# Kernel optimization log

Measured on AMD Instinct MI355X. Metric: run time of the kernel, lower is better.

## Reference

```python
import jax, jax.numpy as jnp
import numpy as np

EPS = 1e-5
STRIDE = 4
NSAMPLE = 8


def _fps(p, m):
    # furthest point sampling on one cloud p:[n,3] -> int32 indices [m]
    d0 = jnp.sum((p - p[0]) ** 2, axis=-1)
    def step(dist, _):
        nxt = jnp.argmax(dist).astype(jnp.int32)
        d = jnp.sum((p - p[nxt]) ** 2, axis=-1)
        return jnp.minimum(dist, d), nxt
    _, idxs = jax.lax.scan(step, d0, None, length=m - 1)
    return jnp.concatenate([jnp.zeros((1,), jnp.int32), idxs])


def _bn(x, gamma, beta):
    # inference-mode BatchNorm1d with running_mean=0, running_var=1
    return gamma * x / jnp.sqrt(1.0 + EPS) + beta


def _transition_down(p, x, W, gamma, beta):
    # p:[B,n,3], x:[B,n,C]  (stride>1 path of TransitionDown)
    B, n, _ = p.shape
    m = n // STRIDE
    pc = jax.lax.stop_gradient(p)
    idx = jax.vmap(_fps, in_axes=(0, None))(pc, m)              # [B,m]
    n_p = jnp.take_along_axis(p, idx[:, :, None], axis=1)       # [B,m,3]
    npc = jax.lax.stop_gradient(n_p)
    # squared distances sampled->all points, [B,m,n] (no [B,m,n,3] temp)
    d2 = (jnp.sum(npc ** 2, -1)[:, :, None]
          + jnp.sum(pc ** 2, -1)[:, None, :]
          - 2.0 * jnp.einsum('bmd,bnd->bmn', npc, pc))
    _, knn = jax.lax.top_k(-d2, NSAMPLE)                        # [B,m,k]
    gp = jax.vmap(lambda pb, kb: pb[kb])(p, knn)                # [B,m,k,3]
    gx = jax.vmap(lambda xb, kb: xb[kb])(x, knn)                # [B,m,k,C]
    rel = gp - n_p[:, :, None, :]                               # use_xyz=True
    feat = jnp.concatenate([rel, gx], axis=-1)                  # [B,m,k,3+C]
    y = jax.nn.relu(_bn(feat @ W, gamma, beta))
    return n_p, jnp.max(y, axis=2)                              # MaxPool1d(k)


def setup_inputs():
    key = jax.random.key(0)
    ks = jax.random.split(key, 16)
    B, n = 8, 8192
    N = B * n
    inp = {
        'p0': jax.random.normal(ks[0], (N, 3), jnp.float32),
        'x0': jax.random.normal(ks[1], (N, 3), jnp.float32),
        'o0': (jnp.arange(1, B + 1) * n).astype(jnp.int32),
    }
    dims_in = [6, 3 + 32, 3 + 64, 3 + 128, 3 + 256]
    dims_out = [32, 64, 128, 256, 512]
    for i in range(5):
        s = 1.0 / np.sqrt(dims_in[i])
        inp[f'W{i+1}'] = jax.random.uniform(ks[2 + i], (dims_in[i], dims_out[i]), jnp.float32, -s, s)
        inp[f'g{i+1}'] = jnp.ones((dims_out[i],), jnp.float32)
        inp[f'b{i+1}'] = jnp.zeros((dims_out[i],), jnp.float32)
    s1 = 1.0 / np.sqrt(512.0)
    inp['Wc1'] = jax.random.uniform(ks[8], (512, 256), jnp.float32, -s1, s1)
    inp['bc1'] = jax.random.uniform(ks[9], (256,), jnp.float32, -s1, s1)
    inp['gcls'] = jnp.ones((256,), jnp.float32)
    inp['bcls'] = jnp.zeros((256,), jnp.float32)
    s2 = 1.0 / np.sqrt(256.0)
    inp['Wc2'] = jax.random.uniform(ks[10], (256, 40), jnp.float32, -s2, s2)
    inp['bc2'] = jax.random.uniform(ks[11], (40,), jnp.float32, -s2, s2)
    return inp


def reference(p0, x0, o0, W1, g1, b1, W2, g2, b2, W3, g3, b3, W4, g4, b4,
              W5, g5, b5, Wc1, bc1, gcls, bcls, Wc2, bc2):
    B = o0.shape[0]
    n = p0.shape[0] // B  # equal-size segments
    p = p0.reshape(B, n, 3)
    x = jnp.concatenate([p0, x0], axis=1).reshape(B, n, 6)  # c=6: cat(xyz, feat)
    # enc1: stride 1 -> relu(bn(linear(x)))
    x = jax.nn.relu(_bn(x @ W1, g1, b1))
    # enc2..enc5: FPS + KNN group + linear/bn/relu + maxpool over neighbors
    p, x = _transition_down(p, x, W2, g2, b2)
    p, x = _transition_down(p, x, W3, g3, b3)
    p, x = _transition_down(p, x, W4, g4, b4)
    p, x = _transition_down(p, x, W5, g5, b5)
    # offset-based segment mean pooling (equal segments -> mean over axis 1)
    pooled = jnp.mean(x, axis=1)                               # [B,512]
    h = jax.nn.relu(_bn(pooled @ Wc1 + bc1, gcls, bcls))       # dropout eval=id
    return h @ Wc2 + bc2                                       # [B,40]
```

## Files before the change

kernel.cpp:

```cpp
#include <hip/hip_runtime.h>
#include <float.h>

#define BNI 0.9999950000374997f

typedef unsigned int v2u __attribute__((ext_vector_type(2)));

__device__ __forceinline__ float sq3(float x, float y, float z) {
  return __fadd_rn(__fadd_rn(__fmul_rn(x, x), __fmul_rn(y, y)), __fmul_rn(z, z));
}

__device__ __forceinline__ int key_idx(double k) { return ~__double2loint(k); }

template <int CTRL>
__device__ __forceinline__ double dpp_max(double k) {
  union { double d; int i[2]; } u, r;
  u.d = k;
  r.i[0] = __builtin_amdgcn_mov_dpp(u.i[0], CTRL, 0xF, 0xF, true);
  r.i[1] = __builtin_amdgcn_mov_dpp(u.i[1], CTRL, 0xF, 0xF, true);
  return fmax(k, r.d);
}
__device__ __forceinline__ double pl16_kmax(double k) {
  union { double d; unsigned i[2]; } u; u.d = k;
  v2u a0 = __builtin_amdgcn_permlane16_swap(u.i[0], u.i[0], false, false);
  v2u a1 = __builtin_amdgcn_permlane16_swap(u.i[1], u.i[1], false, false);
  k = fmax(k, __hiloint2double((int)a1[0], (int)a0[0]));
  k = fmax(k, __hiloint2double((int)a1[1], (int)a0[1]));
  return k;
}
__device__ __forceinline__ double pl32_kmax(double k) {
  union { double d; unsigned i[2]; } u; u.d = k;
  v2u a0 = __builtin_amdgcn_permlane32_swap(u.i[0], u.i[0], false, false);
  v2u a1 = __builtin_amdgcn_permlane32_swap(u.i[1], u.i[1], false, false);
  k = fmax(k, __hiloint2double((int)a1[0], (int)a0[0]));
  k = fmax(k, __hiloint2double((int)a1[1], (int)a0[1]));
  return k;
}
__device__ __forceinline__ double wave_max_key(double k) {
  k = dpp_max<0xB1>(k);
  k = dpp_max<0x4E>(k);
  k = dpp_max<0x141>(k);
  k = dpp_max<0x140>(k);
  k = pl16_kmax(k);
  k = pl32_kmax(k);
  return k;
}

__global__ void k_prep(const float* __restrict__ p, float4* __restrict__ P4, int N) {
  int i = blockIdx.x * blockDim.x + threadIdx.x;
  if (i < N) {
    float x = p[3 * i], y = p[3 * i + 1], z = p[3 * i + 2];
    P4[i] = make_float4(x, y, z, sq3(x, y, z));
  }
}

__device__ __forceinline__ unsigned mpart3(unsigned x) {
  return (x & 1u) | ((x & 2u) << 2) | ((x & 4u) << 4);
}
__device__ __forceinline__ int cell_id(float4 v, const float* __restrict__ bb) {
  int cx = min(max((int)((v.x - bb[0]) * bb[3]), 0), 7);
  int cy = min(max((int)((v.y - bb[1]) * bb[4]), 0), 7);
  int cz = min(max((int)((v.z - bb[2]) * bb[5]), 0), 7);
  return (int)((mpart3(cx) << 2) | (mpart3(cy) << 1) | mpart3(cz));
}

__global__ __launch_bounds__(256) void k_bbox(const float4* __restrict__ P, int n,
                                              float* __restrict__ bb) {
  __shared__ float sm[6][4];
  int b = blockIdx.x, tid = threadIdx.x, lane = tid & 63, wid = tid >> 6;
  const float4* Pb = P + (size_t)b * n;
  float lx = FLT_MAX, hx = -FLT_MAX, ly = FLT_MAX, hy = -FLT_MAX, lz = FLT_MAX, hz = -FLT_MAX;
  for (int i = tid; i < n; i += 256) {
    float4 v = Pb[i];
    lx = fminf(lx, v.x); hx = fmaxf(hx, v.x);
    ly = fminf(ly, v.y); hy = fmaxf(hy, v.y);
    lz = fminf(lz, v.z); hz = fmaxf(hz, v.z);
  }
#pragma unroll
  for (int off = 1; off < 64; off <<= 1) {
    lx = fminf(lx, __shfl_xor(lx, off)); hx = fmaxf(hx, __shfl_xor(hx, off));
    ly = fminf(ly, __shfl_xor(ly, off)); hy = fmaxf(hy, __shfl_xor(hy, off));
    lz = fminf(lz, __shfl_xor(lz, off)); hz = fmaxf(hz, __shfl_xor(hz, off));
  }
  if (lane == 0) {
    sm[0][wid] = lx; sm[1][wid] = hx; sm[2][wid] = ly;
    sm[3][wid] = hy; sm[4][wid] = lz; sm[5][wid] = hz;
  }
  __syncthreads();
  if (tid == 0) {
    float LX = fminf(fminf(sm[0][0], sm[0][1]), fminf(sm[0][2], sm[0][3]));
    float HX = fmaxf(fmaxf(sm[1][0], sm[1][1]), fmaxf(sm[1][2], sm[1][3]));
    float LY = fminf(fminf(sm[2][0], sm[2][1]), fminf(sm[2][2], sm[2][3]));
    float HY = fmaxf(fmaxf(sm[3][0], sm[3][1]), fmaxf(sm[3][2], sm[3][3]));
    float LZ = fminf(fminf(sm[4][0], sm[4][1]), fminf(sm[4][2], sm[4][3]));
    float HZ = fmaxf(fmaxf(sm[5][0], sm[5][1]), fmaxf(sm[5][2], sm[5][3]));
    float ex = HX - LX, ey = HY - LY, ez = HZ - LZ;
    float* o = bb + b * 8;
    o[0] = LX; o[1] = LY; o[2] = LZ;
    o[3] = ex > 0.f ? 8.f / ex : 0.f;
    o[4] = ey > 0.f ? 8.f / ey : 0.f;
    o[5] = ez > 0.f ? 8.f / ez : 0.f;
  }
}

__global__ void k_hist(const float4* __restrict__ P, const float* __restrict__ bb,
                       int* __restrict__ hist, int n, int total) {
  int i = blockIdx.x * blockDim.x + threadIdx.x;
  if (i >= total) return;
  int b = i / n;
  int cid = cell_id(P[i], bb + b * 8);
  atomicAdd(&hist[b * 512 + cid], 1);
}

__global__ __launch_bounds__(512) void k_scan(const int* __restrict__ hist,
                                              int* __restrict__ cursor) {
  __shared__ int s[512];
  int b = blockIdx.x, t = threadIdx.x;
  int h = hist[b * 512 + t];
  s[t] = h;
  __syncthreads();
  for (int d = 1; d < 512; d <<= 1) {
    int v = (t >= d) ? s[t - d] : 0;
    __syncthreads();
    s[t] += v;
    __syncthreads();
  }
  cursor[b * 512 + t] = s[t] - h;
}

__global__ void k_scatter(const float4* __restrict__ P, const float* __restrict__ bb,
                          int* __restrict__ cursor, float4* __restrict__ Psort,
                          int n, int total) {
  int i = blockIdx.x * blockDim.x + threadIdx.x;
  if (i >= total) return;
  int b = i / n, il = i - b * n;
  float4 v = P[i];
  int cid = cell_id(v, bb + b * 8);
  int pos = atomicAdd(&cursor[b * 512 + cid], 1);
  Psort[(size_t)b * n + pos] = make_float4(v.x, v.y, v.z, __int_as_float(il));
}

template <int PT, int NW>
__device__ __forceinline__ void fps_body(
    const float4* __restrict__ Psort, const float4* __restrict__ Porig,
    int n, int m, int* __restrict__ out_idx, int b, double* keys ,
    float4* sQ) {
  const int tid = threadIdx.x;
  const int lane = tid & 63, wid = tid >> 6;
  const float4* PS = Psort + (size_t)b * n;
  const float4* PO = Porig + (size_t)b * n;

  float px[PT], py[PT], pz[PT], dist[PT];
  int ni[PT];
  const int base = wid * (64 * PT);
#pragma unroll
  for (int k = 0; k < PT; ++k) {
    float4 v = PS[base + k * 64 + lane];
    px[k] = v.x; py[k] = v.y; pz[k] = v.z;
    int oi = __float_as_int(v.w);
    ni[k] = ~oi;
    sQ[oi] = make_float4(v.x, v.y, v.z, 0.f);
  }
  float lx = px[0], hx = px[0], ly = py[0], hy = py[0], lz = pz[0], hz = pz[0];
#pragma unroll
  for (int k = 1; k < PT; ++k) {
    lx = fminf(lx, px[k]); hx = fmaxf(hx, px[k]);
    ly = fminf(ly, py[k]); hy = fmaxf(hy, py[k]);
    lz = fminf(lz, pz[k]); hz = fmaxf(hz, pz[k]);
  }
#pragma unroll
  for (int off = 1; off < 64; off <<= 1) {
    lx = fminf(lx, __shfl_xor(lx, off)); hx = fmaxf(hx, __shfl_xor(hx, off));
    ly = fminf(ly, __shfl_xor(ly, off)); hy = fmaxf(hy, __shfl_xor(hy, off));
    lz = fminf(lz, __shfl_xor(lz, off)); hz = fmaxf(hz, __shfl_xor(hz, off));
  }
  if (tid == 0) out_idx[(size_t)b * m] = 0;

  float4 q0 = PO[0];
  double ck[PT];
#pragma unroll
  for (int k = 0; k < PT; ++k) {
    float d = sq3(__fsub_rn(px[k], q0.x), __fsub_rn(py[k], q0.y), __fsub_rn(pz[k], q0.z));
    dist[k] = d;
    ck[k] = __hiloint2double(__float_as_int(d), ni[k]);
  }
#pragma unroll
  for (int s = 1; s < PT; s <<= 1)
#pragma unroll
    for (int k = 0; k + s < PT; k += 2 * s) ck[k] = fmax(ck[k], ck[k + s]);
  double wkey = wave_max_key(ck[0]);

  for (int t = 1; t < m; ++t) {
    int buf = t & 1;
    if (lane == 0) keys[buf * 16 + wid] = wkey;
    __syncthreads();
    double kb = keys[buf * 16 + (lane & (NW - 1))];
    if (NW >= 2)  kb = dpp_max<0xB1>(kb);
    if (NW >= 4)  kb = dpp_max<0x4E>(kb);
    if (NW >= 8)  kb = dpp_max<0x141>(kb);
    if (NW >= 16) kb = dpp_max<0x140>(kb);
    int wi = key_idx(kb);
    if (tid == 0) out_idx[(size_t)b * m + t] = wi;
    if (t + 1 >= m) break;
    float4 qq = sQ[wi];
    float tx = fmaxf(fmaxf(__fsub_rn(lx, qq.x), __fsub_rn(qq.x, hx)), 0.f);
    float ty = fmaxf(fmaxf(__fsub_rn(ly, qq.y), __fsub_rn(qq.y, hy)), 0.f);
    float tz = fmaxf(fmaxf(__fsub_rn(lz, qq.z), __fsub_rn(qq.z, hz)), 0.f);
    float lb = sq3(tx, ty, tz);
    float wv = __uint_as_float((unsigned)__double2hiint(wkey));
    if (lb < wv) {
      double ck2[PT];
#pragma unroll
      for (int k = 0; k < PT; ++k) {
        float d = sq3(__fsub_rn(px[k], qq.x), __fsub_rn(py[k], qq.y), __fsub_rn(pz[k], qq.z));
        float nd = fminf(dist[k], d);
        dist[k] = nd;
        ck2[k] = __hiloint2double(__float_as_int(nd), ni[k]);
      }
#pragma unroll
      for (int s = 1; s < PT; s <<= 1)
#pragma unroll
        for (int k = 0; k + s < PT; k += 2 * s) ck2[k] = fmax(ck2[k], ck2[k + s]);
      wkey = wave_max_key(ck2[0]);
    }
  }
}

__device__ __forceinline__ void enc1_body(
    const float* __restrict__ p0, const float* __restrict__ x0,
    const float* __restrict__ W, const float* __restrict__ g,
    const float* __restrict__ bt, float* __restrict__ X, int N, int t) {
  int pt = t >> 5, c = t & 31;
  if (pt >= N) return;
  float i0 = p0[pt * 3], i1 = p0[pt * 3 + 1], i2 = p0[pt * 3 + 2];
  float i3 = x0[pt * 3], i4 = x0[pt * 3 + 1], i5 = x0[pt * 3 + 2];
  float a = i0 * W[c] + i1 * W[32 + c] + i2 * W[64 + c] +
            i3 * W[96 + c] + i4 * W[128 + c] + i5 * W[160 + c];
  a = a * (g[c] * BNI) + bt[c];
  X[(size_t)pt * 32 + c] = fmaxf(a, 0.f);
}

__device__ void knn_body(const float4* __restrict__ Pq, const float4* __restrict__ Pc,
                         int n, int m, int* __restrict__ knn, int gw) {
  int lane = threadIdx.x & 63;
  int b = gw / m;
  float4 q = Pq[gw];
  const float4* C = Pc + (size_t)b * n;
  float ad[8];
  int ai[8];
#pragma unroll
  for (int s = 0; s < 8; ++s) { ad[s] = FLT_MAX; ai[s] = 0x7fffffff; }
  for (int j = lane; j < n; j += 64) {
    float4 c = C[j];
    float dot = __fadd_rn(__fadd_rn(__fmul_rn(q.x, c.x), __fmul_rn(q.y, c.y)), __fmul_rn(q.z, c.z));
    float d2 = __fsub_rn(__fadd_rn(q.w, c.w), __fmul_rn(2.f, dot));
    if (d2 < ad[7] || (d2 == ad[7] && j < ai[7])) {
      float cd = d2; int ci = j;
#pragma unroll
      for (int s = 0; s < 8; ++s) {
        bool sw = (cd < ad[s]) || (cd == ad[s] && ci < ai[s]);
        float td = ad[s]; int ti = ai[s];
        ad[s] = sw ? cd : td; ai[s] = sw ? ci : ti;
        cd = sw ? td : cd;  ci = sw ? ti : ci;
      }
    }
  }
  int pos = 0;
  int* kout = knn + (size_t)gw * 8;
#pragma unroll
  for (int r = 0; r < 8; ++r) {
    float hv = FLT_MAX; int hi = 0x7fffffff;
#pragma unroll
    for (int s = 7; s >= 0; --s)
      if (pos == s) { hv = ad[s]; hi = ai[s]; }
    float v = hv; int ix = hi;
#pragma unroll
    for (int off = 1; off < 64; off <<= 1) {
      float ov = __shfl_xor(v, off);
      int oi = __shfl_xor(ix, off);
      if (ov < v || (ov == v && oi < ix)) { v = ov; ix = oi; }
    }
    if (hv == v && hi == ix) pos++;
    if (lane == 0) kout[r] = ix;
  }
}

template <int CINF, int COUT, int NT>
__device__ __forceinline__ void feat_body(
    const float4* __restrict__ Pq, const float4* __restrict__ Pc,
    const float* __restrict__ Xin, const int* __restrict__ knn,
    const float* __restrict__ W, const float* __restrict__ g,
    const float* __restrict__ bt, float* __restrict__ Xout,
    int n, int m, int bi0, int total, char* smem) {
  constexpr int F = 3 + CINF;
  constexpr int NQ = NT / COUT;
  typedef float SF[8][F];
  SF* sf = (SF*)smem;
  int tid = threadIdx.x;
  if (tid < NQ * 8) {
    int ql = tid >> 3, k = tid & 7;
    int bi = bi0 + ql;
    if (bi < total) {
      float4 q = Pq[bi];
      int b = bi / m;
      int nb = knn[(size_t)bi * 8 + k];
      float4 c = Pc[(size_t)b * n + nb];
      sf[ql][k][0] = c.x - q.x;
      sf[ql][k][1] = c.y - q.y;
      sf[ql][k][2] = c.z - q.z;
    }
  }
  for (int e = tid; e < NQ * 8 * CINF; e += NT) {
    int ql = e / (8 * CINF);
    int r = e - ql * (8 * CINF);
    int k = r / CINF, j = r - k * CINF;
    int bi = bi0 + ql;
    if (bi < total) {
      int b = bi / m;
      int nb = knn[(size_t)bi * 8 + k];
      sf[ql][k][3 + j] = Xin[((size_t)b * n + nb) * CINF + j];
    }
  }
  __syncthreads();
  int ql = tid / COUT, c = tid - ql * COUT;
  int bi = bi0 + ql;
  if (bi >= total) return;
  float acc[8] = {0.f, 0.f, 0.f, 0.f, 0.f, 0.f, 0.f, 0.f};
  for (int j = 0; j < F; ++j) {
    float w = W[(size_t)j * COUT + c];
#pragma unroll
    for (int k = 0; k < 8; ++k) acc[k] = fmaf(sf[ql][k][j], w, acc[k]);
  }
  float sc = g[c] * BNI, bb = bt[c];
  float mx = 0.f;
#pragma unroll
  for (int k = 0; k < 8; ++k) mx = fmaxf(mx, fmaf(acc[k], sc, bb));
  Xout[(size_t)bi * COUT + c] = mx;
}

__global__ __launch_bounds__(1024) void k_combo0(
    const float4* __restrict__ Psort, const float4* __restrict__ P2,
    int n, int m2, int* __restrict__ fpsI,
    const float* __restrict__ p0, const float* __restrict__ x0,
    const float* __restrict__ W1, const float* __restrict__ g1,
    const float* __restrict__ b1, float* __restrict__ X1, int N, int B) {
  __shared__ double skeys[32];
  __shared__ float4 sQ[8192];
  int bid = blockIdx.x;
  if (bid < B) { fps_body<8, 16>(Psort, P2, n, m2, fpsI, bid, skeys, sQ); return; }
  enc1_body(p0, x0, W1, g1, b1, X1, N, (bid - B) * 1024 + threadIdx.x);
}

__global__ __launch_bounds__(512) void k_combo1(
    const float4* __restrict__ Psort, const float4* __restrict__ P3,
    int m2, int m3, int* __restrict__ fpsI,
    const float4* __restrict__ P2, int n, int* __restrict__ knnA,
    int B, int totq) {
  __shared__ double skeys[32];
  __shared__ float4 sQ[2048];
  int bid = blockIdx.x;
  if (bid < B) { fps_body<4, 8>(Psort, P3, m2, m3, fpsI, bid, skeys, sQ); return; }
  int gw = (bid - B) * 8 + (threadIdx.x >> 6);
  if (gw < totq) knn_body(P3, P2, n, m2, knnA, gw);
}

__global__ __launch_bounds__(256) void k_combo2(
    const float4* __restrict__ Psort, const float4* __restrict__ P4s,
    int m3, int m4, int* __restrict__ fpsI,
    const float4* __restrict__ P3, int m2, int* __restrict__ knnB,
    const float4* __restrict__ P2, const float* __restrict__ X1,
    const int* __restrict__ knnA,
    const float* __restrict__ W2, const float* __restrict__ g2,
    const float* __restrict__ b2, float* __restrict__ X2,
    int n, int B, int nkb, int totq3, int totq2) {
  __shared__ double skeys[32];
  __shared__ float4 sQ[512];
  __shared__ __align__(16) char sfm[4480];
  int bid = blockIdx.x;
  if (bid < B) { fps_body<2, 4>(Psort, P4s, m3, m4, fpsI, bid, skeys, sQ); return; }
  bid -= B;
  if (bid < nkb) {
    int gw = bid * 4 + (threadIdx.x >> 6);
    if (gw < totq3) knn_body(P4s, P3, m2, m3, knnB, gw);
    return;
  }
  bid -= nkb;
  feat_body<32, 64, 256>(P3, P2, X1, knnA, W2, g2, b2, X2, n, m2,
                         bid * 4, totq2, sfm);
}

__global__ __launch_bounds__(128) void k_combo3(
    const float4* __restrict__ Psort, const float4* __restrict__ P5,
    int m4, int m5, int* __restrict__ fpsI,
    const float4* __restrict__ P4s, int m3, int* __restrict__ knnA,
    const float4* __restrict__ P3, const float* __restrict__ X2,
    const int* __restrict__ knnB,
    const float* __restrict__ W3, const float* __restrict__ g3,
    const float* __restrict__ b3, float* __restrict__ X3,
    int m2, int B, int nkb, int totq4, int totq3) {
  __shared__ double skeys[32];
  __shared__ float4 sQ[128];
  __shared__ __align__(16) char sfm[2144];
  int bid = blockIdx.x;
  if (bid < B) { fps_body<1, 2>(Psort, P5, m4, m5, fpsI, bid, skeys, sQ); return; }
  bid -= B;
  if (bid < nkb) {
    int gw = bid * 2 + (threadIdx.x >> 6);
    if (gw < totq4) knn_body(P5, P4s, m3, m4, knnA, gw);
    return;
  }
  bid -= nkb;
  feat_body<64, 128, 128>(P4s, P3, X2, knnB, W3, g3, b3, X3, m2, m3,
                          bid, totq3, sfm);
}

__global__ __launch_bounds__(512) void k_combo4(
    const float4* __restrict__ P6, const float4* __restrict__ P5,
    int m4, int m5, int* __restrict__ knnB,
    const float4* __restrict__ P4s, const float* __restrict__ X3,
    const int* __restrict__ knnA,
    const float* __restrict__ W4, const float* __restrict__ g4,
    const float* __restrict__ b4, float* __restrict__ X4,
    int m3, int nkb, int totq5, int totq4) {
  __shared__ __align__(16) char sfm[8384];
  int bid = blockIdx.x;
  if (bid < nkb) {
    int gw = bid * 8 + (threadIdx.x >> 6);
    if (gw < totq5) knn_body(P6, P5, m4, m5, knnB, gw);
    return;
  }
  bid -= nkb;
  feat_body<128, 256, 512>(P5, P4s, X3, knnA, W4, g4, b4, X4, m3, m4,
                           bid * 2, totq4, sfm);
}

__global__ void k_gather(const float4* __restrict__ Pin, const int* __restrict__ idx,
                         float4* __restrict__ Pout, int n, int m, int total) {
  int t = blockIdx.x * blockDim.x + threadIdx.x;
  if (t >= total) return;
  int b = t / m;
  Pout[t] = Pin[(size_t)b * n + idx[t]];
}

__global__ __launch_bounds__(512) void k_feat5(
    const float4* __restrict__ Pq, const float4* __restrict__ Pc,
    const float* __restrict__ Xin, const int* __restrict__ knn,
    const float* __restrict__ W, const float* __restrict__ g,
    const float* __restrict__ bt, float* __restrict__ Xout, int n, int m) {
  __shared__ __align__(16) char sfm[8 * 259 * 4];
  feat_body<256, 512, 512>(Pq, Pc, Xin, knn, W, g, bt, Xout, n, m,
                           blockIdx.x, gridDim.x, sfm);
}

__global__ __launch_bounds__(512) void k_head(
    const float* __restrict__ X5, const float* __restrict__ Wc1, const float* __restrict__ bc1,
    const float* __restrict__ gc, const float* __restrict__ bcl,
    const float* __restrict__ Wc2, const float* __restrict__ bc2,
    float* __restrict__ out, int m5) {
  __shared__ float sp[512];
  __shared__ float sh[256];
  int b = blockIdx.x, tid = threadIdx.x;
  float s = 0.f;
  for (int i = 0; i < m5; ++i) s += X5[((size_t)b * m5 + i) * 512 + tid];
  sp[tid] = s * (1.0f / m5);
  __syncthreads();
  if (tid < 256) {
    float a = bc1[tid];
    for (int j = 0; j < 512; ++j) a = fmaf(sp[j], Wc1[j * 256 + tid], a);
    a = a * (gc[tid] * BNI) + bcl[tid];
    sh[tid] = fmaxf(a, 0.f);
  }
  __syncthreads();
  if (tid < 40) {
    float a = bc2[tid];
    for (int j = 0; j < 256; ++j) a = fmaf(sh[j], Wc2[j * 40 + tid], a);
    out[b * 40 + tid] = a;
  }
}

extern "C" void kernel_launch(void* const* d_in, const int* in_sizes, int n_in,
                              void* d_out, int out_size, void* d_ws, size_t ws_size,
                              hipStream_t stream) {
  const float* p0 = (const float*)d_in[0];
  const float* x0 = (const float*)d_in[1];
  const int B = in_sizes[2];
  const int N = in_sizes[0] / 3;
  const int n = N / B;
  const float* W1 = (const float*)d_in[3];
  const float* g1 = (const float*)d_in[4];
  const float* b1 = (const float*)d_in[5];
  const float* W2 = (const float*)d_in[6];
  const float* g2 = (const float*)d_in[7];
  const float* b2 = (const float*)d_in[8];
  const float* W3 = (const float*)d_in[9];
  const float* g3 = (const float*)d_in[10];
  const float* b3 = (const float*)d_in[11];
  const float* W4 = (const float*)d_in[12];
  const float* g4 = (const float*)d_in[13];
  const float* b4 = (const float*)d_in[14];
  const float* W5 = (const float*)d_in[15];
  const float* g5 = (const float*)d_in[16];
  const float* b5 = (const float*)d_in[17];
  const float* Wc1 = (const float*)d_in[18];
  const float* bc1 = (const float*)d_in[19];
  const float* gcls = (const float*)d_in[20];
  const float* bcls = (const float*)d_in[21];
  const float* Wc2 = (const float*)d_in[22];
  const float* bc2 = (const float*)d_in[23];
  float* out = (float*)d_out;

  const int m2 = n / 4, m3 = m2 / 4, m4 = m3 / 4, m5 = m4 / 4;

  char* ws = (char*)d_ws;
  size_t off = 0;
  auto alloc = [&](size_t bytes) -> void* {
    void* p = ws + off;
    off += (bytes + 255) & ~(size_t)255;
    return p;
  };
  float4* P2 = (float4*)alloc((size_t)N * 16);
  float* X1 = (float*)alloc((size_t)N * 32 * 4);
  float4* P3 = (float4*)alloc((size_t)B * m2 * 16);
  float4* P4s = (float4*)alloc((size_t)B * m3 * 16);
  float4* P5 = (float4*)alloc((size_t)B * m4 * 16);
  float4* P6 = (float4*)alloc((size_t)B * m5 * 16);
  int* fpsI = (int*)alloc((size_t)B * m2 * 4);
  int* knnA = (int*)alloc((size_t)B * m2 * 8 * 4);
  int* knnB = (int*)alloc((size_t)B * m3 * 8 * 4);
  float* X2 = (float*)alloc((size_t)B * m2 * 64 * 4);
  float* X3 = (float*)alloc((size_t)B * m3 * 128 * 4);
  float* X4 = (float*)alloc((size_t)B * m4 * 256 * 4);
  float* X5 = (float*)alloc((size_t)B * m5 * 512 * 4);
  float4* Psort = (float4*)alloc((size_t)N * 16);
  float* bbox = (float*)alloc((size_t)B * 8 * 4);
  int* hist = (int*)alloc((size_t)B * 512 * 4);
  int* cursor = (int*)alloc((size_t)B * 512 * 4);

  auto sort_stage = [&](const float4* P, int ns) {
    int total = B * ns;
    hipMemsetAsync(hist, 0, (size_t)B * 512 * 4, stream);
    k_bbox<<<B, 256, 0, stream>>>(P, ns, bbox);
    k_hist<<<(total + 255) / 256, 256, 0, stream>>>(P, bbox, hist, ns, total);
    k_scan<<<B, 512, 0, stream>>>(hist, cursor);
    k_scatter<<<(total + 255) / 256, 256, 0, stream>>>(P, bbox, cursor, Psort, ns, total);
  };

  k_prep<<<(N + 255) / 256, 256, 0, stream>>>(p0, P2, N);

  sort_stage(P2, n);
  {
    int eb = (N * 32 + 1023) / 1024;
    k_combo0<<<B + eb, 1024, 0, stream>>>(Psort, P2, n, m2, fpsI,
                                          p0, x0, W1, g1, b1, X1, N, B);
  }
  k_gather<<<(B * m2 + 255) / 256, 256, 0, stream>>>(P2, fpsI, P3, n, m2, B * m2);

  sort_stage(P3, m2);
  {
    int kb = (B * m2 + 7) / 8;
    k_combo1<<<B + kb, 512, 0, stream>>>(Psort, P3, m2, m3, fpsI,
                                         P2, n, knnA, B, B * m2);
  }
  k_gather<<<(B * m3 + 255) / 256, 256, 0, stream>>>(P3, fpsI, P4s, m2, m3, B * m3);

  sort_stage(P4s, m3);
  {
    int nkb = (B * m3 + 3) / 4;
    int fb = (B * m2 + 3) / 4;
    k_combo2<<<B + nkb + fb, 256, 0, stream>>>(
        Psort, P4s, m3, m4, fpsI, P3, m2, knnB, P2, X1, knnA,
        W2, g2, b2, X2, n, B, nkb, B * m3, B * m2);
  }
  k_gather<<<(B * m4 + 255) / 256, 256, 0, stream>>>(P4s, fpsI, P5, m3, m4, B * m4);

  sort_stage(P5, m4);
  {
    int nkb = (B * m4 + 1) / 2;
    int fb = B * m3;
    k_combo3<<<B + nkb + fb, 128, 0, stream>>>(
        Psort, P5, m4, m5, fpsI, P4s, m3, knnA, P3, X2, knnB,
        W3, g3, b3, X3, m2, B, nkb, B * m4, B * m3);
  }
  k_gather<<<(B * m5 + 255) / 256, 256, 0, stream>>>(P5, fpsI, P6, m4, m5, B * m5);

  {
    int nkb = (B * m5 + 7) / 8;
    int fb = (B * m4 + 1) / 2;
    k_combo4<<<nkb + fb, 512, 0, stream>>>(
        P6, P5, m4, m5, knnB, P4s, X3, knnA,
        W4, g4, b4, X4, m3, nkb, B * m5, B * m4);
  }

  k_feat5<<<B * m5, 512, 0, stream>>>(P6, P5, X4, knnB, W5, g5, b5, X5, m4, m5);
  k_head<<<B, 512, 0, stream>>>(X5, Wc1, bc1, gcls, bcls, Wc2, bc2, out, m5);
}
```

Measured before the change: 2.216 ms.

## Fuse gather and grid sort into one per-batch kernel; pass FPS coords via readlane

Replaces the gather plus memset/bbox/hist/scan/scatter kernel chain with a single per-batch kernel that does the gather, bounding box, histogram, scan and scatter in shared memory. This removes many small kernel launches and global atomics per stage. FPS also publishes each wave's winning coordinates with its key, so the next query point is picked with a ballot and readlane instead of a dependent shared-memory lookup, shortening the serial per-iteration latency. The risk is that the 8-block sort for the full cloud has low parallelism.

```diff
diff --git a/kernel.cpp b/kernel.cpp
--- a/kernel.cpp
+++ b/kernel.cpp
@@ -10,6 +10,10 @@
 }
 
 __device__ __forceinline__ int key_idx(double k) { return ~__double2loint(k); }
+
+__device__ __forceinline__ float rdlane_f(float v, int l) {
+  return __int_as_float(__builtin_amdgcn_readlane(__float_as_int(v), l));
+}
 
 template <int CTRL>
 __device__ __forceinline__ double dpp_max(double k) {
@@ -56,21 +60,39 @@
 __device__ __forceinline__ unsigned mpart3(unsigned x) {
   return (x & 1u) | ((x & 2u) << 2) | ((x & 4u) << 4);
 }
-__device__ __forceinline__ int cell_id(float4 v, const float* __restrict__ bb) {
+__device__ __forceinline__ int cell_id(float4 v, const float* bb) {
   int cx = min(max((int)((v.x - bb[0]) * bb[3]), 0), 7);
   int cy = min(max((int)((v.y - bb[1]) * bb[4]), 0), 7);
   int cz = min(max((int)((v.z - bb[2]) * bb[5]), 0), 7);
   return (int)((mpart3(cx) << 2) | (mpart3(cy) << 1) | mpart3(cz));
 }
 
-__global__ __launch_bounds__(256) void k_bbox(const float4* __restrict__ P, int n,
-                                              float* __restrict__ bb) {
-  __shared__ float sm[6][4];
-  int b = blockIdx.x, tid = threadIdx.x, lane = tid & 63, wid = tid >> 6;
-  const float4* Pb = P + (size_t)b * n;
+template <int NPTS, bool DOGATHER>
+__global__ __launch_bounds__(1024) void k_sortgather(
+    const float4* __restrict__ Pin, const int* __restrict__ fpsI, int n_prev,
+    float4* __restrict__ Pout, float4* __restrict__ Psort) {
+  __shared__ float4 sPts[NPTS];
+  __shared__ int sHist[512], sScan[512], sCur[512];
+  __shared__ float sBB[6][16];
+  __shared__ float sBBf[8];
+  const int b = blockIdx.x, tid = threadIdx.x;
+  const int lane = tid & 63, wid = tid >> 6;
+  for (int i = tid; i < NPTS; i += 1024) {
+    float4 v;
+    if (DOGATHER) {
+      int src = fpsI[(size_t)b * NPTS + i];
+      v = Pin[(size_t)b * n_prev + src];
+      Pout[(size_t)b * NPTS + i] = v;
+    } else {
+      v = Pin[(size_t)b * NPTS + i];
+    }
+    sPts[i] = v;
+  }
+  if (tid < 512) sHist[tid] = 0;
+  __syncthreads();
   float lx = FLT_MAX, hx = -FLT_MAX, ly = FLT_MAX, hy = -FLT_MAX, lz = FLT_MAX, hz = -FLT_MAX;
-  for (int i = tid; i < n; i += 256) {
-    float4 v = Pb[i];
+  for (int i = tid; i < NPTS; i += 1024) {
+    float4 v = sPts[i];
     lx = fminf(lx, v.x); hx = fmaxf(hx, v.x);
     ly = fminf(ly, v.y); hy = fmaxf(hy, v.y);
     lz = fminf(lz, v.z); hz = fmaxf(hz, v.z);
@@ -82,68 +104,50 @@
     lz = fminf(lz, __shfl_xor(lz, off)); hz = fmaxf(hz, __shfl_xor(hz, off));
   }
   if (lane == 0) {
-    sm[0][wid] = lx; sm[1][wid] = hx; sm[2][wid] = ly;
-    sm[3][wid] = hy; sm[4][wid] = lz; sm[5][wid] = hz;
+    sBB[0][wid] = lx; sBB[1][wid] = hx; sBB[2][wid] = ly;
+    sBB[3][wid] = hy; sBB[4][wid] = lz; sBB[5][wid] = hz;
   }
   __syncthreads();
   if (tid == 0) {
-    float LX = fminf(fminf(sm[0][0], sm[0][1]), fminf(sm[0][2], sm[0][3]));
-    float HX = fmaxf(fmaxf(sm[1][0], sm[1][1]), fmaxf(sm[1][2], sm[1][3]));
-    float LY = fminf(fminf(sm[2][0], sm[2][1]), fminf(sm[2][2], sm[2][3]));
-    float HY = fmaxf(fmaxf(sm[3][0], sm[3][1]), fmaxf(sm[3][2], sm[3][3]));
-    float LZ = fminf(fminf(sm[4][0], sm[4][1]), fminf(sm[4][2], sm[4][3]));
-    float HZ = fmaxf(fmaxf(sm[5][0], sm[5][1]), fmaxf(sm[5][2], sm[5][3]));
+    float LX = FLT_MAX, HX = -FLT_MAX, LY = FLT_MAX, HY = -FLT_MAX, LZ = FLT_MAX, HZ = -FLT_MAX;
+    for (int w = 0; w < 16; ++w) {
+      LX = fminf(LX, sBB[0][w]); HX = fmaxf(HX, sBB[1][w]);
+      LY = fminf(LY, sBB[2][w]); HY = fmaxf(HY, sBB[3][w]);
+      LZ = fminf(LZ, sBB[4][w]); HZ = fmaxf(HZ, sBB[5][w]);
+    }
     float ex = HX - LX, ey = HY - LY, ez = HZ - LZ;
-    float* o = bb + b * 8;
-    o[0] = LX; o[1] = LY; o[2] = LZ;
-    o[3] = ex > 0.f ? 8.f / ex : 0.f;
-    o[4] = ey > 0.f ? 8.f / ey : 0.f;
-    o[5] = ez > 0.f ? 8.f / ez : 0.f;
-  }
-}
-
-__global__ void k_hist(const float4* __restrict__ P, const float* __restrict__ bb,
-                       int* __restrict__ hist, int n, int total) {
-  int i = blockIdx.x * blockDim.x + threadIdx.x;
-  if (i >= total) return;
-  int b = i / n;
-  int cid = cell_id(P[i], bb + b * 8);
-  atomicAdd(&hist[b * 512 + cid], 1);
-}
-
-__global__ __launch_bounds__(512) void k_scan(const int* __restrict__ hist,
-                                              int* __restrict__ cursor) {
-  __shared__ int s[512];
-  int b = blockIdx.x, t = threadIdx.x;
-  int h = hist[b * 512 + t];
-  s[t] = h;
+    sBBf[0] = LX; sBBf[1] = LY; sBBf[2] = LZ;
+    sBBf[3] = ex > 0.f ? 8.f / ex : 0.f;
+    sBBf[4] = ey > 0.f ? 8.f / ey : 0.f;
+    sBBf[5] = ez > 0.f ? 8.f / ez : 0.f;
+  }
+  __syncthreads();
+  for (int i = tid; i < NPTS; i += 1024)
+    atomicAdd(&sHist[cell_id(sPts[i], sBBf)], 1);
+  __syncthreads();
+  if (tid < 512) sScan[tid] = sHist[tid];
   __syncthreads();
   for (int d = 1; d < 512; d <<= 1) {
-    int v = (t >= d) ? s[t - d] : 0;
+    int v = 0;
+    if (tid < 512 && tid >= d) v = sScan[tid - d];
     __syncthreads();
-    s[t] += v;
+    if (tid < 512) sScan[tid] += v;
     __syncthreads();
   }
-  cursor[b * 512 + t] = s[t] - h;
-}
-
-__global__ void k_scatter(const float4* __restrict__ P, const float* __restrict__ bb,
-                          int* __restrict__ cursor, float4* __restrict__ Psort,
-                          int n, int total) {
-  int i = blockIdx.x * blockDim.x + threadIdx.x;
-  if (i >= total) return;
-  int b = i / n, il = i - b * n;
-  float4 v = P[i];
-  int cid = cell_id(v, bb + b * 8);
-  int pos = atomicAdd(&cursor[b * 512 + cid], 1);
-  Psort[(size_t)b * n + pos] = make_float4(v.x, v.y, v.z, __int_as_float(il));
+  if (tid < 512) sCur[tid] = sScan[tid] - sHist[tid];
+  __syncthreads();
+  for (int i = tid; i < NPTS; i += 1024) {
+    float4 v = sPts[i];
+    int pos = atomicAdd(&sCur[cell_id(v, sBBf)], 1);
+    Psort[(size_t)b * NPTS + pos] = make_float4(v.x, v.y, v.z, __int_as_float(i));
+  }
 }
 
 template <int PT, int NW>
 __device__ __forceinline__ void fps_body(
     const float4* __restrict__ Psort, const float4* __restrict__ Porig,
-    int n, int m, int* __restrict__ out_idx, int b, double* keys ,
-    float4* sQ) {
+    int n, int m, int* __restrict__ out_idx, int b,
+    double* skey , float4* scrd , float4* sQ) {
   const int tid = threadIdx.x;
   const int lane = tid & 63, wid = tid >> 6;
   const float4* PS = Psort + (size_t)b * n;
@@ -188,30 +192,37 @@
 #pragma unroll
     for (int k = 0; k + s < PT; k += 2 * s) ck[k] = fmax(ck[k], ck[k + s]);
   double wkey = wave_max_key(ck[0]);
+  __syncthreads();
+  float4 myc = sQ[key_idx(wkey)];
 
   for (int t = 1; t < m; ++t) {
     int buf = t & 1;
-    if (lane == 0) keys[buf * 16 + wid] = wkey;
+    if (lane == 0) { skey[buf * 16 + wid] = wkey; scrd[buf * 16 + wid] = myc; }
     __syncthreads();
-    double kb = keys[buf * 16 + (lane & (NW - 1))];
-    if (NW >= 2)  kb = dpp_max<0xB1>(kb);
-    if (NW >= 4)  kb = dpp_max<0x4E>(kb);
-    if (NW >= 8)  kb = dpp_max<0x141>(kb);
-    if (NW >= 16) kb = dpp_max<0x140>(kb);
-    int wi = key_idx(kb);
-    if (tid == 0) out_idx[(size_t)b * m + t] = wi;
+    int rs = lane & (NW - 1);
+    double mine = skey[buf * 16 + rs];
+    float4 pc = scrd[buf * 16 + rs];
+    double ckk = mine;
+    if (NW >= 2)  ckk = dpp_max<0xB1>(ckk);
+    if (NW >= 4)  ckk = dpp_max<0x4E>(ckk);
+    if (NW >= 8)  ckk = dpp_max<0x141>(ckk);
+    if (NW >= 16) ckk = dpp_max<0x140>(ckk);
+    if (tid == 0) out_idx[(size_t)b * m + t] = key_idx(ckk);
     if (t + 1 >= m) break;
-    float4 qq = sQ[wi];
-    float tx = fmaxf(fmaxf(__fsub_rn(lx, qq.x), __fsub_rn(qq.x, hx)), 0.f);
-    float ty = fmaxf(fmaxf(__fsub_rn(ly, qq.y), __fsub_rn(qq.y, hy)), 0.f);
-    float tz = fmaxf(fmaxf(__fsub_rn(lz, qq.z), __fsub_rn(qq.z, hz)), 0.f);
+    unsigned long long bal =
+        __ballot(__double_as_longlong(mine) == __double_as_longlong(ckk));
+    int w = (int)__ffsll((long long)bal) - 1;
+    float qx = rdlane_f(pc.x, w), qy = rdlane_f(pc.y, w), qz = rdlane_f(pc.z, w);
+    float tx = fmaxf(fmaxf(__fsub_rn(lx, qx), __fsub_rn(qx, hx)), 0.f);
+    float ty = fmaxf(fmaxf(__fsub_rn(ly, qy), __fsub_rn(qy, hy)), 0.f);
+    float tz = fmaxf(fmaxf(__fsub_rn(lz, qz), __fsub_rn(qz, hz)), 0.f);
     float lb = sq3(tx, ty, tz);
     float wv = __uint_as_float((unsigned)__double2hiint(wkey));
     if (lb < wv) {
       double ck2[PT];
 #pragma unroll
       for (int k = 0; k < PT; ++k) {
-        float d = sq3(__fsub_rn(px[k], qq.x), __fsub_rn(py[k], qq.y), __fsub_rn(pz[k], qq.z));
+        float d = sq3(__fsub_rn(px[k], qx), __fsub_rn(py[k], qy), __fsub_rn(pz[k], qz));
         float nd = fminf(dist[k], d);
         dist[k] = nd;
         ck2[k] = __hiloint2double(__float_as_int(nd), ni[k]);
@@ -221,6 +232,7 @@
 #pragma unroll
         for (int k = 0; k + s < PT; k += 2 * s) ck2[k] = fmax(ck2[k], ck2[k + s]);
       wkey = wave_max_key(ck2[0]);
+      myc = sQ[key_idx(wkey)];
     }
   }
 }
@@ -344,9 +356,10 @@
     const float* __restrict__ W1, const float* __restrict__ g1,
     const float* __restrict__ b1, float* __restrict__ X1, int N, int B) {
   __shared__ double skeys[32];
+  __shared__ float4 scrds[32];
   __shared__ float4 sQ[8192];
   int bid = blockIdx.x;
-  if (bid < B) { fps_body<8, 16>(Psort, P2, n, m2, fpsI, bid, skeys, sQ); return; }
+  if (bid < B) { fps_body<8, 16>(Psort, P2, n, m2, fpsI, bid, skeys, scrds, sQ); return; }
   enc1_body(p0, x0, W1, g1, b1, X1, N, (bid - B) * 1024 + threadIdx.x);
 }
 
@@ -356,9 +369,10 @@
     const float4* __restrict__ P2, int n, int* __restrict__ knnA,
     int B, int totq) {
   __shared__ double skeys[32];
+  __shared__ float4 scrds[32];
   __shared__ float4 sQ[2048];
   int bid = blockIdx.x;
-  if (bid < B) { fps_body<4, 8>(Psort, P3, m2, m3, fpsI, bid, skeys, sQ); return; }
+  if (bid < B) { fps_body<4, 8>(Psort, P3, m2, m3, fpsI, bid, skeys, scrds, sQ); return; }
   int gw = (bid - B) * 8 + (threadIdx.x >> 6);
   if (gw < totq) knn_body(P3, P2, n, m2, knnA, gw);
 }
@@ -373,10 +387,11 @@
     const float* __restrict__ b2, float* __restrict__ X2,
     int n, int B, int nkb, int totq3, int totq2) {
   __shared__ double skeys[32];
+  __shared__ float4 scrds[32];
   __shared__ float4 sQ[512];
   __shared__ __align__(16) char sfm[4480];
   int bid = blockIdx.x;
-  if (bid < B) { fps_body<2, 4>(Psort, P4s, m3, m4, fpsI, bid, skeys, sQ); return; }
+  if (bid < B) { fps_body<2, 4>(Psort, P4s, m3, m4, fpsI, bid, skeys, scrds, sQ); return; }
   bid -= B;
   if (bid < nkb) {
     int gw = bid * 4 + (threadIdx.x >> 6);
@@ -398,10 +413,11 @@
     const float* __restrict__ b3, float* __restrict__ X3,
     int m2, int B, int nkb, int totq4, int totq3) {
   __shared__ double skeys[32];
+  __shared__ float4 scrds[32];
   __shared__ float4 sQ[128];
   __shared__ __align__(16) char sfm[2144];
   int bid = blockIdx.x;
-  if (bid < B) { fps_body<1, 2>(Psort, P5, m4, m5, fpsI, bid, skeys, sQ); return; }
+  if (bid < B) { fps_body<1, 2>(Psort, P5, m4, m5, fpsI, bid, skeys, scrds, sQ); return; }
   bid -= B;
   if (bid < nkb) {
     int gw = bid * 2 + (threadIdx.x >> 6);
@@ -531,38 +547,24 @@
   float* X4 = (float*)alloc((size_t)B * m4 * 256 * 4);
   float* X5 = (float*)alloc((size_t)B * m5 * 512 * 4);
   float4* Psort = (float4*)alloc((size_t)N * 16);
-  float* bbox = (float*)alloc((size_t)B * 8 * 4);
-  int* hist = (int*)alloc((size_t)B * 512 * 4);
-  int* cursor = (int*)alloc((size_t)B * 512 * 4);
-
-  auto sort_stage = [&](const float4* P, int ns) {
-    int total = B * ns;
-    hipMemsetAsync(hist, 0, (size_t)B * 512 * 4, stream);
-    k_bbox<<<B, 256, 0, stream>>>(P, ns, bbox);
-    k_hist<<<(total + 255) / 256, 256, 0, stream>>>(P, bbox, hist, ns, total);
-    k_scan<<<B, 512, 0, stream>>>(hist, cursor);
-    k_scatter<<<(total + 255) / 256, 256, 0, stream>>>(P, bbox, cursor, Psort, ns, total);
-  };
 
   k_prep<<<(N + 255) / 256, 256, 0, stream>>>(p0, P2, N);
 
-  sort_stage(P2, n);
+  k_sortgather<8192, false><<<B, 1024, 0, stream>>>(P2, nullptr, 0, nullptr, Psort);
   {
     int eb = (N * 32 + 1023) / 1024;
     k_combo0<<<B + eb, 1024, 0, stream>>>(Psort, P2, n, m2, fpsI,
                                           p0, x0, W1, g1, b1, X1, N, B);
   }
-  k_gather<<<(B * m2 + 255) / 256, 256, 0, stream>>>(P2, fpsI, P3, n, m2, B * m2);
-
-  sort_stage(P3, m2);
+
+  k_sortgather<2048, true><<<B, 1024, 0, stream>>>(P2, fpsI, n, P3, Psort);
   {
     int kb = (B * m2 + 7) / 8;
     k_combo1<<<B + kb, 512, 0, stream>>>(Psort, P3, m2, m3, fpsI,
                                          P2, n, knnA, B, B * m2);
   }
-  k_gather<<<(B * m3 + 255) / 256, 256, 0, stream>>>(P3, fpsI, P4s, m2, m3, B * m3);
-
-  sort_stage(P4s, m3);
+
+  k_sortgather<512, true><<<B, 1024, 0, stream>>>(P3, fpsI, m2, P4s, Psort);
   {
     int nkb = (B * m3 + 3) / 4;
     int fb = (B * m2 + 3) / 4;
@@ -570,9 +572,8 @@
         Psort, P4s, m3, m4, fpsI, P3, m2, knnB, P2, X1, knnA,
         W2, g2, b2, X2, n, B, nkb, B * m3, B * m2);
   }
-  k_gather<<<(B * m4 + 255) / 256, 256, 0, stream>>>(P4s, fpsI, P5, m3, m4, B * m4);
-
-  sort_stage(P5, m4);
+
+  k_sortgather<128, true><<<B, 1024, 0, stream>>>(P4s, fpsI, m3, P5, Psort);
   {
     int nkb = (B * m4 + 1) / 2;
     int fb = B * m3;
```

Measured after the change: 2.382 ms. 1.07x slower.
